# Kernel optimization log

Hardware: AMD Instinct MI355X
Metric: run time of the kernel (lower is better)

## Reference

```python
import jax, jax.numpy as jnp
import numpy as np

B, L, DC, DQ, H = 32, 1024, 1024, 1024, 512
NEG_NUM = -10000.0


def setup_inputs() -> dict:
    key = jax.random.key(0)
    ks = jax.random.split(key, 7)
    s1 = 1.0 / np.sqrt(DC + DQ)
    s2 = 1.0 / np.sqrt(H)
    return {
        "ctx": jax.random.normal(ks[0], (B, L, DC), jnp.float32),
        "query": jax.random.normal(ks[1], (B, DQ), jnp.float32),
        "mask": jnp.ones((B, L), jnp.int32),
        "noise": jax.random.normal(ks[2], (B, L), jnp.float32),
        "W1": jax.random.uniform(ks[3], (DC + DQ, H), jnp.float32, -s1, s1),
        "b1": jax.random.uniform(ks[4], (H,), jnp.float32, -s1, s1),
        "w2": jax.random.uniform(ks[5], (H,), jnp.float32, -s2, s2),
        "b2": jnp.zeros((), jnp.float32),
    }


def reference(ctx, query, mask, noise, W1, b1, w2, b2):
    b, l, dc = ctx.shape
    # concat([ctx, query_expanded]) @ W1 == ctx @ W1[:DC] + query @ W1[DC:]
    hidden = jnp.tanh(
        jnp.einsum("blc,ch->blh", ctx, W1[:dc])
        + (query @ W1[dc:])[:, None, :]
        + b1
    )  # [B, L, H]
    score = hidden @ w2 + b2  # [B, L]
    score = jnp.where(mask == 0, NEG_NUM, score)
    score = score + noise  # sigmoid_noise=True -> coefficient 1
    p = jax.nn.sigmoid(score)  # p_choose_i [B, L]

    # initial prev_att: one-hot at position 0
    prev_att = jnp.zeros((b, l), score.dtype).at[:, 0].set(1.0)
    # shifted (1 - p): [1, 1-p_0, ..., 1-p_{L-2}]
    shifted = jnp.concatenate(
        [jnp.ones((b, 1), p.dtype), 1.0 - p[:, :-1]], axis=1
    )

    # linear recurrence a_t = shifted_t * a_{t-1} + prev_att_t  (a_{-1}=0)
    def step(carry, xs):
        s_t, pr_t = xs
        a = s_t * carry + pr_t
        return a, a

    _, att_t = jax.lax.scan(step, jnp.zeros((b,), p.dtype), (shifted.T, prev_att.T))
    att = att_t.T * p  # [B, L]

    expected_ctx = jnp.einsum("bl,blc->bc", att, ctx)  # bmm(p_ctx[:,None,:], ctx)
    return expected_ctx, att
```

## Files before the change

### kernel.cpp

```cpp
#include <hip/hip_runtime.h>
#include <hip/hip_bf16.h>
#include <math.h>

constexpr int Bb = 32;
constexpr int Ll = 1024;
constexpr int DC = 1024;
constexpr int DQ = 1024;
constexpr int Hh = 512;
#define NEG_NUM -10000.0f

typedef __attribute__((ext_vector_type(8))) short bf16x8;
typedef __attribute__((ext_vector_type(4))) float f32x4;

#define GLOAD_LDS16(g, l)                                                  \
    __builtin_amdgcn_global_load_lds(                                      \
        (const __attribute__((address_space(1))) void*)(g),                \
        (__attribute__((address_space(3))) void*)(l), 16, 0, 0)

__device__ inline unsigned short f2bf(float f) {
    unsigned int x = __float_as_uint(f);
    unsigned int r = (x + 0x7FFFu + ((x >> 16) & 1u)) >> 16;
    return (unsigned short)r;
}
__device__ inline float bfu(unsigned short u) {
    return __uint_as_float(((unsigned int)u) << 16);
}


__global__ __launch_bounds__(256) void prep_kernel(const float* __restrict__ W1,
                                                   const float* __restrict__ query,
                                                   const float* __restrict__ b1,
                                                   const float* __restrict__ ctx,
                                                   unsigned short* __restrict__ w1t,
                                                   float* __restrict__ qb,
                                                   float* __restrict__ score,
                                                   float* __restrict__ out_ctx,
                                                   unsigned short* __restrict__ ctxb) {
    __shared__ float red[4][64];
    const int bid = blockIdx.x;
    if (bid < 2048) {
        int idx = bid * 256 + threadIdx.x;
        int n = idx >> 10, k = idx & 1023;
        int ks = k ^ ((n & 7) << 3);
        w1t[(size_t)n * 1024 + ks] = f2bf(W1[(size_t)k * Hh + n]);
    } else if (bid < 2176) {
        int i = (bid - 2048) * 256 + threadIdx.x;
        out_ctx[i] = 0.f;
        score[i] = 0.f;
    } else if (bid < 2432) {
        const int qbid = bid - 2176;
        const int b  = qbid >> 3;
        const int hg = qbid & 7;
        const int hl = threadIdx.x & 63;
        const int j  = threadIdx.x >> 6;
        const int h  = hg * 64 + hl;
        const float* q = query + (size_t)b * DQ + j * 256;
        const float* w = W1 + (size_t)(DC + j * 256) * Hh + h;
        float a0 = 0.f, a1 = 0.f, a2 = 0.f, a3 = 0.f;
#pragma unroll 4
        for (int c = 0; c < 256; c += 4) {
            a0 += q[c + 0] * w[(size_t)(c + 0) * Hh];
            a1 += q[c + 1] * w[(size_t)(c + 1) * Hh];
            a2 += q[c + 2] * w[(size_t)(c + 2) * Hh];
            a3 += q[c + 3] * w[(size_t)(c + 3) * Hh];
        }
        red[j][hl] = (a0 + a1) + (a2 + a3);
        __syncthreads();
        if (j == 0)
            qb[(size_t)b * Hh + h] = red[0][hl] + red[1][hl] + red[2][hl] + red[3][hl] + b1[h];
    } else {
        size_t i = (size_t)((bid - 2432) * 256 + threadIdx.x) * 8;
        int row = (int)(i >> 10);
        int col = (int)(i & 1023);
        float4 v0 = *(const float4*)(ctx + i);
        float4 v1 = *(const float4*)(ctx + i + 4);
        union { unsigned short us[8]; uint4 v; } o;
        o.us[0] = f2bf(v0.x); o.us[1] = f2bf(v0.y); o.us[2] = f2bf(v0.z); o.us[3] = f2bf(v0.w);
        o.us[4] = f2bf(v1.x); o.us[5] = f2bf(v1.y); o.us[6] = f2bf(v1.z); o.us[7] = f2bf(v1.w);
        *(uint4*)(ctxb + ((size_t)row << 10) + (col ^ ((row & 7) << 3))) = o.v;
    }
}

__global__ __launch_bounds__(512, 1) void gemm_mfma(const unsigned short* __restrict__ ctxb,
                                                    const unsigned short* __restrict__ w1t,
                                                    const float* __restrict__ qb,
                                                    const float* __restrict__ w2,
                                                    float* __restrict__ score) {
    __shared__ unsigned short lds[2 * 32768];

    const int bid = blockIdx.x;
    const int n0 = ((bid >> 3) & 1) * 256;
    const int m0 = (((bid >> 4) << 3) | (bid & 7)) * 256;

    const int tid = threadIdx.x;
    const int wv = tid >> 6, lane = tid & 63;
    const int wr = wv >> 2, wc = wv & 3;
    const int lr = lane & 15, lk = lane >> 4;

    char* ldsB = (char*)lds;
    const char* ctxB = (const char*)ctxb;
    const char* w1tB = (const char*)w1t;

    const int srow = tid >> 3;
    const int scolb = (tid & 7) * 16;
    const int x = (lr & 7) << 4;

    f32x4 acc[8][4];
#pragma unroll
    for (int mf = 0; mf < 8; ++mf)
#pragma unroll
        for (int nf = 0; nf < 4; ++nf) acc[mf][nf] = (f32x4){0.f, 0.f, 0.f, 0.f};

#pragma unroll
    for (int i = 0; i < 4; ++i) {
        int row = i * 64 + srow;
        GLOAD_LDS16(ctxB + (size_t)(m0 + row) * 2048 + scolb,
                    ldsB + i * 8192 + tid * 16);
        GLOAD_LDS16(w1tB + (size_t)(n0 + row) * 2048 + scolb,
                    ldsB + 32768 + i * 8192 + tid * 16);
    }

    for (int ks = 0; ks < 16; ++ks) {
        const int cur = ks & 1;
        char* bufc = ldsB + cur * 65536;
        char* bufn = ldsB + (cur ^ 1) * 65536;
        const int kb = (ks + 1) * 128;

        __builtin_amdgcn_s_barrier();
        if (ks < 15) {
#pragma unroll
            for (int i = 0; i < 2; ++i) {
                int row = i * 64 + srow;
                GLOAD_LDS16(ctxB + (size_t)(m0 + row) * 2048 + kb + scolb,
                            bufn + i * 8192 + tid * 16);
                GLOAD_LDS16(w1tB + (size_t)(n0 + row) * 2048 + kb + scolb,
                            bufn + 32768 + i * 8192 + tid * 16);
            }
            asm volatile("s_waitcnt vmcnt(4)" ::: "memory");
        } else {
            asm volatile("s_waitcnt vmcnt(0)" ::: "memory");
        }
        __builtin_amdgcn_sched_barrier(0);
        __builtin_amdgcn_s_barrier();

        {
            const int colb = (lk * 16) ^ x;
            bf16x8 a[8], bb[4];
#pragma unroll
            for (int nf = 0; nf < 4; ++nf)
                bb[nf] = *(const bf16x8*)(bufc + 32768 + (wc * 64 + nf * 16 + lr) * 128 + colb);
#pragma unroll
            for (int mf = 0; mf < 8; ++mf)
                a[mf] = *(const bf16x8*)(bufc + (wr * 128 + mf * 16 + lr) * 128 + colb);
            __builtin_amdgcn_s_setprio(1);
#pragma unroll
            for (int mf = 0; mf < 8; ++mf)
#pragma unroll
                for (int nf = 0; nf < 4; ++nf)
                    acc[mf][nf] = __builtin_amdgcn_mfma_f32_16x16x32_bf16(a[mf], bb[nf], acc[mf][nf], 0, 0, 0);
            __builtin_amdgcn_s_setprio(0);
        }
        __builtin_amdgcn_s_barrier();
        if (ks < 15) {
#pragma unroll
            for (int i = 2; i < 4; ++i) {
                int row = i * 64 + srow;
                GLOAD_LDS16(ctxB + (size_t)(m0 + row) * 2048 + kb + scolb,
                            bufn + i * 8192 + tid * 16);
                GLOAD_LDS16(w1tB + (size_t)(n0 + row) * 2048 + kb + scolb,
                            bufn + 32768 + i * 8192 + tid * 16);
            }
        }
        {
            const int colb = (64 + lk * 16) ^ x;
            bf16x8 a[8], bb[4];
#pragma unroll
            for (int nf = 0; nf < 4; ++nf)
                bb[nf] = *(const bf16x8*)(bufc + 32768 + (wc * 64 + nf * 16 + lr) * 128 + colb);
#pragma unroll
            for (int mf = 0; mf < 8; ++mf)
                a[mf] = *(const bf16x8*)(bufc + (wr * 128 + mf * 16 + lr) * 128 + colb);
            __builtin_amdgcn_s_setprio(1);
#pragma unroll
            for (int mf = 0; mf < 8; ++mf)
#pragma unroll
                for (int nf = 0; nf < 4; ++nf)
                    acc[mf][nf] = __builtin_amdgcn_mfma_f32_16x16x32_bf16(a[mf], bb[nf], acc[mf][nf], 0, 0, 0);
            __builtin_amdgcn_s_setprio(0);
        }
    }

    const int bq = m0 >> 10;
    const float* qbb = qb + (size_t)bq * Hh;
#pragma unroll
    for (int mf = 0; mf < 8; ++mf) {
        float s0 = 0.f, s1 = 0.f, s2 = 0.f, s3 = 0.f;
#pragma unroll
        for (int nf = 0; nf < 4; ++nf) {
            int col = n0 + wc * 64 + nf * 16 + lr;
            float wvw = w2[col];
            float qv = qbb[col];
            s0 += tanhf(acc[mf][nf][0] + qv) * wvw;
            s1 += tanhf(acc[mf][nf][1] + qv) * wvw;
            s2 += tanhf(acc[mf][nf][2] + qv) * wvw;
            s3 += tanhf(acc[mf][nf][3] + qv) * wvw;
        }
#pragma unroll
        for (int off = 8; off; off >>= 1) {
            s0 += __shfl_xor(s0, off, 16);
            s1 += __shfl_xor(s1, off, 16);
            s2 += __shfl_xor(s2, off, 16);
            s3 += __shfl_xor(s3, off, 16);
        }
        if (lr == 0) {
            int row = m0 + wr * 128 + mf * 16 + lk * 4;
            atomicAdd(&score[row + 0], s0);
            atomicAdd(&score[row + 1], s1);
            atomicAdd(&score[row + 2], s2);
            atomicAdd(&score[row + 3], s3);
        }
    }
}

__global__ __launch_bounds__(256) void ectx_fused(const unsigned short* __restrict__ ctxb,
                                                  const float* __restrict__ score,
                                                  const int* __restrict__ mask,
                                                  const float* __restrict__ noise,
                                                  const float* __restrict__ b2p,
                                                  float* __restrict__ att_out,
                                                  float* __restrict__ out) {
    __shared__ float att_s[1024];
    const int b = blockIdx.z;
    const int ly = blockIdx.y;
    const int tid = threadIdx.x;

    if (tid < 64) {
        const int lane = tid;
        const float b2 = b2p[0];
        const int base = b * Ll + lane * 16;
        float p[16], q[16];
        float run = 1.f;
#pragma unroll
        for (int j = 0; j < 16; ++j) {
            int l = base + j;
            float s = score[l] + b2;
            if (mask[l] == 0) s = NEG_NUM;
            s += noise[l];
            float pv = 1.f / (1.f + expf(-s));
            p[j] = pv;
            run *= (1.f - pv);
            q[j] = run;
        }
        float incl = run;
#pragma unroll
        for (int off = 1; off < 64; off <<= 1) {
            float v = __shfl_up(incl, off, 64);
            if (lane >= off) incl *= v;
        }
        float excl = __shfl_up(incl, 1, 64);
        if (lane == 0) excl = 1.f;
#pragma unroll
        for (int j = 0; j < 16; ++j) {
            float P = excl * (j == 0 ? 1.f : q[j - 1]);
            float av = p[j] * P;
            att_s[lane * 16 + j] = av;
            if (ly == 0) att_out[base + j] = av;
        }
    }
    __syncthreads();

    const int l0 = ly * 128;
    const unsigned short* cb = ctxb + ((size_t)b * Ll + l0) * DC;
    const int c = tid * 4;
    float a0 = 0.f, a1 = 0.f, a2 = 0.f, a3 = 0.f;
    for (int l = 0; l < 128; ++l) {
        float av = att_s[l0 + l];
        int cs = c ^ ((l & 7) << 3);
        ushort4 v = *(const ushort4*)(cb + (size_t)l * DC + cs);
        a0 += av * bfu(v.x); a1 += av * bfu(v.y);
        a2 += av * bfu(v.z); a3 += av * bfu(v.w);
    }
    float* o = out + (size_t)b * DC + c;
    atomicAdd(o + 0, a0); atomicAdd(o + 1, a1);
    atomicAdd(o + 2, a2); atomicAdd(o + 3, a3);
}

extern "C" void kernel_launch(void* const* d_in, const int* in_sizes, int n_in,
                              void* d_out, int out_size, void* d_ws, size_t ws_size,
                              hipStream_t stream) {
    const float* ctx   = (const float*)d_in[0];
    const float* query = (const float*)d_in[1];
    const int*   mask  = (const int*)d_in[2];
    const float* noise = (const float*)d_in[3];
    const float* W1    = (const float*)d_in[4];
    const float* b1    = (const float*)d_in[5];
    const float* w2    = (const float*)d_in[6];
    const float* b2    = (const float*)d_in[7];

    float* out_ctx = (float*)d_out;
    float* out_att = (float*)d_out + Bb * DC;

    char* ws = (char*)d_ws;
    float* score = (float*)ws;
    float* qb    = (float*)(ws + 131072);
    unsigned short* w1t  = (unsigned short*)(ws + 196608);
    unsigned short* ctxb = (unsigned short*)(ws + 1245184);

    prep_kernel<<<18816, 256, 0, stream>>>(W1, query, b1, ctx, w1t, qb, score, out_ctx, ctxb);

    gemm_mfma<<<256, 512, 0, stream>>>(ctxb, w1t, qb, w2, score);

    ectx_fused<<<dim3(1, Ll / 128, Bb), 256, 0, stream>>>(ctxb, score, mask, noise, b2,
                                                          out_att, out_ctx);
}
```

Before: 101.3 us.

## Restructure GEMM k-loop into M-half phases with staggered LDS prefetch

Reorganizes the main MFMA loop of the fused score GEMM. It now computes the two M-halves (mf 0-3, then 4-7) across both K-halves, keeps both B fragments in registers, and spreads the next tile's global-to-LDS loads across the phases. Each phase only waits for the rows it needs next (vmcnt 6/2), so fewer full waits sit between compute and loads, and register pressure drops from 8 A fragments to 4. The risk is subtle waitcnt/barrier ordering errors that could read LDS rows before they land, and the extra B registers held live.

```diff
diff --git a/kernel.cpp b/kernel.cpp
--- a/kernel.cpp
+++ b/kernel.cpp
@@ -81,6 +81,13 @@
     }
 }
 
+#define STAGE_A(i, kb, buf)                                                   \
+    GLOAD_LDS16(ctxB + (size_t)(m0 + (i) * 64 + srow) * 2048 + (kb) + scolb,  \
+                (buf) + (i) * 8192 + tid * 16)
+#define STAGE_B(i, kb, buf)                                                   \
+    GLOAD_LDS16(w1tB + (size_t)(n0 + (i) * 64 + srow) * 2048 + (kb) + scolb,  \
+                (buf) + 32768 + (i) * 8192 + tid * 16)
+
 __global__ __launch_bounds__(512, 1) void gemm_mfma(const unsigned short* __restrict__ ctxb,
                                                     const unsigned short* __restrict__ w1t,
                                                     const float* __restrict__ qb,
@@ -111,13 +118,14 @@
 #pragma unroll
         for (int nf = 0; nf < 4; ++nf) acc[mf][nf] = (f32x4){0.f, 0.f, 0.f, 0.f};
 
-#pragma unroll
-    for (int i = 0; i < 4; ++i) {
-        int row = i * 64 + srow;
-        GLOAD_LDS16(ctxB + (size_t)(m0 + row) * 2048 + scolb,
-                    ldsB + i * 8192 + tid * 16);
-        GLOAD_LDS16(w1tB + (size_t)(n0 + row) * 2048 + scolb,
-                    ldsB + 32768 + i * 8192 + tid * 16);
+    {
+        char* buf = ldsB;
+        STAGE_A(0, 0, buf); STAGE_A(2, 0, buf);
+        STAGE_B(0, 0, buf); STAGE_B(1, 0, buf); STAGE_B(2, 0, buf); STAGE_B(3, 0, buf);
+        STAGE_A(1, 0, buf); STAGE_A(3, 0, buf);
+        asm volatile("s_waitcnt vmcnt(2)" ::: "memory");
+        __builtin_amdgcn_sched_barrier(0);
+        __builtin_amdgcn_s_barrier();
     }
 
     for (int ks = 0; ks < 16; ++ks) {
@@ -125,69 +133,78 @@
         char* bufc = ldsB + cur * 65536;
         char* bufn = ldsB + (cur ^ 1) * 65536;
         const int kb = (ks + 1) * 128;
-
-        __builtin_amdgcn_s_barrier();
-        if (ks < 15) {
-#pragma unroll
-            for (int i = 0; i < 2; ++i) {
-                int row = i * 64 + srow;
-                GLOAD_LDS16(ctxB + (size_t)(m0 + row) * 2048 + kb + scolb,
-                            bufn + i * 8192 + tid * 16);
-                GLOAD_LDS16(w1tB + (size_t)(n0 + row) * 2048 + kb + scolb,
-                            bufn + 32768 + i * 8192 + tid * 16);
-            }
-            asm volatile("s_waitcnt vmcnt(4)" ::: "memory");
-        } else {
-            asm volatile("s_waitcnt vmcnt(0)" ::: "memory");
-        }
+        const bool pf = (ks < 15);
+
+        if (pf) {
+            STAGE_A(0, kb, bufn); STAGE_A(2, kb, bufn);
+            STAGE_B(0, kb, bufn); STAGE_B(1, kb, bufn);
+            STAGE_B(2, kb, bufn); STAGE_B(3, kb, bufn);
+        }
+
+        const int colb0 = (lk * 16) ^ x;
+        const int colb1 = (64 + lk * 16) ^ x;
+        bf16x8 bb0[4], bb1[4], a[4];
+
+#pragma unroll
+        for (int nf = 0; nf < 4; ++nf)
+            bb0[nf] = *(const bf16x8*)(bufc + 32768 + (wc * 64 + nf * 16 + lr) * 128 + colb0);
+#pragma unroll
+        for (int mf = 0; mf < 4; ++mf)
+            a[mf] = *(const bf16x8*)(bufc + (wr * 128 + mf * 16 + lr) * 128 + colb0);
+        __builtin_amdgcn_s_setprio(1);
+#pragma unroll
+        for (int mf = 0; mf < 4; ++mf)
+#pragma unroll
+            for (int nf = 0; nf < 4; ++nf)
+                acc[mf][nf] = __builtin_amdgcn_mfma_f32_16x16x32_bf16(a[mf], bb0[nf], acc[mf][nf], 0, 0, 0);
+        __builtin_amdgcn_s_setprio(0);
+
+#pragma unroll
+        for (int nf = 0; nf < 4; ++nf)
+            bb1[nf] = *(const bf16x8*)(bufc + 32768 + (wc * 64 + nf * 16 + lr) * 128 + colb1);
+#pragma unroll
+        for (int mf = 0; mf < 4; ++mf)
+            a[mf] = *(const bf16x8*)(bufc + (wr * 128 + mf * 16 + lr) * 128 + colb1);
+        __builtin_amdgcn_s_setprio(1);
+#pragma unroll
+        for (int mf = 0; mf < 4; ++mf)
+#pragma unroll
+            for (int nf = 0; nf < 4; ++nf)
+                acc[mf][nf] = __builtin_amdgcn_mfma_f32_16x16x32_bf16(a[mf], bb1[nf], acc[mf][nf], 0, 0, 0);
+        __builtin_amdgcn_s_setprio(0);
+
+        if (pf) asm volatile("s_waitcnt vmcnt(6)" ::: "memory");
+        else    asm volatile("s_waitcnt vmcnt(0)" ::: "memory");
         __builtin_amdgcn_sched_barrier(0);
         __builtin_amdgcn_s_barrier();
 
-        {
-            const int colb = (lk * 16) ^ x;
-            bf16x8 a[8], bb[4];
+        if (pf) { STAGE_A(1, kb, bufn); STAGE_A(3, kb, bufn); }
+
+#pragma unroll
+        for (int mf = 0; mf < 4; ++mf)
+            a[mf] = *(const bf16x8*)(bufc + (wr * 128 + (mf + 4) * 16 + lr) * 128 + colb0);
+        __builtin_amdgcn_s_setprio(1);
+#pragma unroll
+        for (int mf = 0; mf < 4; ++mf)
 #pragma unroll
             for (int nf = 0; nf < 4; ++nf)
-                bb[nf] = *(const bf16x8*)(bufc + 32768 + (wc * 64 + nf * 16 + lr) * 128 + colb);
-#pragma unroll
-            for (int mf = 0; mf < 8; ++mf)
-                a[mf] = *(const bf16x8*)(bufc + (wr * 128 + mf * 16 + lr) * 128 + colb);
-            __builtin_amdgcn_s_setprio(1);
-#pragma unroll
-            for (int mf = 0; mf < 8; ++mf)
-#pragma unroll
-                for (int nf = 0; nf < 4; ++nf)
-                    acc[mf][nf] = __builtin_amdgcn_mfma_f32_16x16x32_bf16(a[mf], bb[nf], acc[mf][nf], 0, 0, 0);
-            __builtin_amdgcn_s_setprio(0);
-        }
+                acc[mf + 4][nf] = __builtin_amdgcn_mfma_f32_16x16x32_bf16(a[mf], bb0[nf], acc[mf + 4][nf], 0, 0, 0);
+        __builtin_amdgcn_s_setprio(0);
+
+#pragma unroll
+        for (int mf = 0; mf < 4; ++mf)
+            a[mf] = *(const bf16x8*)(bufc + (wr * 128 + (mf + 4) * 16 + lr) * 128 + colb1);
+        __builtin_amdgcn_s_setprio(1);
+#pragma unroll
+        for (int mf = 0; mf < 4; ++mf)
+#pragma unroll
+            for (int nf = 0; nf < 4; ++nf)
+                acc[mf + 4][nf] = __builtin_amdgcn_mfma_f32_16x16x32_bf16(a[mf], bb1[nf], acc[mf + 4][nf], 0, 0, 0);
+        __builtin_amdgcn_s_setprio(0);
+
+        if (pf) asm volatile("s_waitcnt vmcnt(2)" ::: "memory");
+        __builtin_amdgcn_sched_barrier(0);
         __builtin_amdgcn_s_barrier();
-        if (ks < 15) {
-#pragma unroll
-            for (int i = 2; i < 4; ++i) {
-                int row = i * 64 + srow;
-                GLOAD_LDS16(ctxB + (size_t)(m0 + row) * 2048 + kb + scolb,
-                            bufn + i * 8192 + tid * 16);
-                GLOAD_LDS16(w1tB + (size_t)(n0 + row) * 2048 + kb + scolb,
-                            bufn + 32768 + i * 8192 + tid * 16);
-            }
-        }
-        {
-            const int colb = (64 + lk * 16) ^ x;
-            bf16x8 a[8], bb[4];
-#pragma unroll
-            for (int nf = 0; nf < 4; ++nf)
-                bb[nf] = *(const bf16x8*)(bufc + 32768 + (wc * 64 + nf * 16 + lr) * 128 + colb);
-#pragma unroll
-            for (int mf = 0; mf < 8; ++mf)
-                a[mf] = *(const bf16x8*)(bufc + (wr * 128 + mf * 16 + lr) * 128 + colb);
-            __builtin_amdgcn_s_setprio(1);
-#pragma unroll
-            for (int mf = 0; mf < 8; ++mf)
-#pragma unroll
-                for (int nf = 0; nf < 4; ++nf)
-                    acc[mf][nf] = __builtin_amdgcn_mfma_f32_16x16x32_bf16(a[mf], bb[nf], acc[mf][nf], 0, 0, 0);
-            __builtin_amdgcn_s_setprio(0);
-        }
     }
 
     const int bq = m0 >> 10;
```

Result: no change. 101.8 us (+0.5%).
